# Performance work log

Hardware: AMD Instinct MI355X
Metric: run time of the kernel (lower is better)

## Reference

```python
import jax, jax.numpy as jnp
import numpy as np

N, E, G = 100000, 3_200_000, 128   # nodes, edges, graphs in batch
IN, H, C = 16, 64, 4               # in_dim, hidden, num_classes


def setup_inputs() -> dict:
    key = jax.random.key(0)
    ks = jax.random.split(key, 6)
    x = jax.random.normal(ks[0], (N, IN), dtype=jnp.float32)
    edge_index = jax.random.randint(ks[1], (2, E), 0, N, dtype=jnp.int64)
    batch = jnp.sort(jax.random.randint(ks[2], (N,), 0, G, dtype=jnp.int64))
    glorot = lambda k, shp, fan: jax.random.normal(k, shp, jnp.float32) / np.sqrt(fan).astype(np.float32)
    return dict(
        x=x, edge_index=edge_index, batch=batch,
        W1=glorot(ks[3], (IN, H), IN), b1=jnp.zeros((H,), jnp.float32),
        W2=glorot(ks[4], (H, H), H), b2=jnp.zeros((H,), jnp.float32),
        Wl=glorot(ks[5], (H, C), H), bl=jnp.zeros((C,), jnp.float32),
    )


def gcn_conv(x, src, dst, W, b, n):
    """PyG GCNConv: h = D^{-1/2} (A+I) D^{-1/2} (x W) + b, edges incl. self-loops."""
    h = x @ W  # [n, out]
    deg = jax.ops.segment_sum(jnp.ones(src.shape[0], x.dtype), dst, num_segments=n)
    dinv = jnp.where(deg > 0, jax.lax.rsqrt(deg), 0.0)
    norm = dinv[src] * dinv[dst]                       # [E+n]
    out = jax.ops.segment_sum(h[src] * norm[:, None], dst, num_segments=n)
    return out + b


def reference(x, edge_index, batch, W1, b1, W2, b2, Wl, bl):
    n = x.shape[0]
    loops = jnp.arange(n, dtype=edge_index.dtype)      # self-loops (gcn_norm)
    src = jnp.concatenate([edge_index[0], loops])
    dst = jnp.concatenate([edge_index[1], loops])
    h = jax.nn.relu(gcn_conv(x, src, dst, W1, b1, n))
    h = jax.nn.relu(gcn_conv(h, src, dst, W2, b2, n))
    g = jax.ops.segment_sum(h, batch, num_segments=G)  # global_add_pool -> [G, H]
    return g @ Wl + bl                                  # [G, C]
```

## Files before the change

kernel.cpp:

```cpp
#include <hip/hip_runtime.h>
#include <hip/hip_bf16.h>

#define NN 100000
#define EE 3200000
#define GG 128
#define IN_DIM 16
#define HDIM 64
#define CDIM 4

#define RN 256
#define NB ((NN + RN - 1) / RN)
#define CH 8192

typedef unsigned short u16;
typedef unsigned int u32;
typedef __attribute__((ext_vector_type(8))) short bf16x8;
typedef __attribute__((ext_vector_type(4))) float f32x4;

__device__ __forceinline__ float bf_lo(u32 w) { return __uint_as_float(w << 16); }
__device__ __forceinline__ float bf_hi(u32 w) { return __uint_as_float(w & 0xFFFF0000u); }
__device__ __forceinline__ u16 f2bf(float f) {
    u32 x = __float_as_uint(f);
    return (u16)((x + 0x7FFFu + ((x >> 16) & 1u)) >> 16);
}
__device__ __forceinline__ float rdlane(float v, int lane) {
    return __int_as_float(__builtin_amdgcn_readlane(__float_as_int(v), lane));
}


__global__ __launch_bounds__(512) void bhist_k(const int* __restrict__ dst,
                                               int* __restrict__ bcnt) {
    __shared__ int hist[NB];
    int t = threadIdx.x;
    long e0 = (long)blockIdx.x * CH;
    int cnt = (int)min((long)CH, (long)EE - e0);
    for (int i = t; i < NB; i += 512) hist[i] = 0;
    __syncthreads();
    for (int i = t; i < cnt; i += 512) atomicAdd(&hist[dst[e0 + i] >> 8], 1);
    __syncthreads();
    for (int i = t; i < NB; i += 512) {
        int v = hist[i];
        if (v > 0) atomicAdd(&bcnt[i], v);
    }
}

__global__ void bucketscan_k(const int* __restrict__ bcnt, int* __restrict__ bucketBase,
                             int* __restrict__ gcursor) {
    __shared__ int s[512];
    int t = threadIdx.x;
    int c = (t < NB) ? bcnt[t] : 0;
    s[t] = c;
    __syncthreads();
    for (int off = 1; off < 512; off <<= 1) {
        int v = (t >= off) ? s[t - off] : 0;
        __syncthreads();
        s[t] += v;
        __syncthreads();
    }
    if (t < NB) {
        int base = s[t] - c;
        bucketBase[t] = base;
        gcursor[t] = base;
    }
    if (t == 0) bucketBase[NB] = EE;
}


__global__ __launch_bounds__(512) void partition_k(const int* __restrict__ src,
                                                   const int* __restrict__ dst,
                                                   int* __restrict__ gcursor,
                                                   u32* __restrict__ pairs) {
    __shared__ int hist[NB];
    __shared__ int lbase[NB];
    __shared__ int gbase[NB];
    __shared__ int scanbuf[512];
    __shared__ u32 stag[CH];
    __shared__ u16 stagb[CH];
    int t = threadIdx.x;
    long e0 = (long)blockIdx.x * CH;
    int cnt = (int)min((long)CH, (long)EE - e0);

    for (int i = t; i < NB; i += 512) hist[i] = 0;
    __syncthreads();

    int myb[16], myloc[16];
    u32 myp[16];
#pragma unroll
    for (int r = 0; r < 16; ++r) {
        int i = t + (r << 9);
        if (i < cnt) {
            int s = src[e0 + i], d = dst[e0 + i];
            int b = d >> 8;
            myb[r] = b;
            myp[r] = ((u32)s << 8) | (u32)(d & 255);
            myloc[r] = atomicAdd(&hist[b], 1);
        } else {
            myb[r] = -1;
            myloc[r] = 0;
            myp[r] = 0;
        }
    }
    __syncthreads();

    scanbuf[t] = (t < NB) ? hist[t] : 0;
    __syncthreads();
    for (int off = 1; off < 512; off <<= 1) {
        int v = (t >= off) ? scanbuf[t - off] : 0;
        __syncthreads();
        scanbuf[t] += v;
        __syncthreads();
    }
    if (t < NB) {
        lbase[t] = scanbuf[t] - hist[t];
        gbase[t] = (hist[t] > 0) ? atomicAdd(&gcursor[t], hist[t]) : 0;
    }
    __syncthreads();

#pragma unroll
    for (int r = 0; r < 16; ++r) {
        if (myb[r] >= 0) {
            int pos = lbase[myb[r]] + myloc[r];
            stag[pos] = myp[r];
            stagb[pos] = (u16)myb[r];
        }
    }
    __syncthreads();

    for (int i = t; i < cnt; i += 512) {
        int b = stagb[i];
        pairs[gbase[b] + (i - lbase[b])] = stag[i];
    }
}


__global__ __launch_bounds__(512) void csrfill_k(const int* __restrict__ bucketBase,
                                                 const u32* __restrict__ pairs,
                                                 int* __restrict__ rowptr,
                                                 float* __restrict__ dinv,
                                                 int* __restrict__ srcS) {
    __shared__ int sb[256];
    __shared__ int sdeg[256];
    __shared__ int lcur[256];
    int b = blockIdx.x, t = threadIdx.x;
    int n0 = b << 8;
    int gb = bucketBase[b];
    int gend = bucketBase[b + 1];

    if (t < 256) sb[t] = 0;
    __syncthreads();

    for (int idx = gb + t; idx < gend; idx += 512) atomicAdd(&sb[pairs[idx] & 255u], 1);
    __syncthreads();

    int d = (t < 256) ? sb[t] : 0;
    if (t < 256) {
        sdeg[t] = d;
        int n = n0 + t;
        if (n < NN) dinv[n] = rsqrtf((float)(d + 1));
    }
    __syncthreads();
    for (int off = 1; off < 256; off <<= 1) {
        int v = 0;
        if (t < 256 && t >= off) v = sb[t - off];
        __syncthreads();
        if (t < 256) sb[t] += v;
        __syncthreads();
    }
    if (t < 256) {
        int excl = sb[t] - sdeg[t];
        int n = n0 + t;
        if (n < NN) rowptr[n] = gb + excl;
        lcur[t] = excl;
    }
    if (b == 0 && t == 0) rowptr[NN] = EE;
    __syncthreads();

    for (int idx = gb + t; idx < gend; idx += 512) {
        u32 p = pairs[idx];
        int dl = (int)(p & 255u);
        int slot = atomicAdd(&lcur[dl], 1);
        srcS[gb + slot] = (int)(p >> 8);
    }
}


__global__ void xs_k(const float* __restrict__ x, const float* __restrict__ dinv,
                     u16* __restrict__ xs) {
    int i = blockIdx.x * 256 + threadIdx.x;
    if (i >= NN * 4) return;
    int n = i >> 2;
    float dn = dinv[n];
    float4 v = ((const float4*)x)[i];
    u32 p0 = (u32)f2bf(v.x * dn) | ((u32)f2bf(v.y * dn) << 16);
    u32 p1 = (u32)f2bf(v.z * dn) | ((u32)f2bf(v.w * dn) << 16);
    uint2 pk; pk.x = p0; pk.y = p1;
    ((uint2*)xs)[i] = pk;
}

#define ACCUM8(acc, v)                       \
    {                                        \
        acc[0] += bf_lo(v.x);                \
        acc[1] += bf_hi(v.x);                \
        acc[2] += bf_lo(v.y);                \
        acc[3] += bf_hi(v.y);                \
        acc[4] += bf_lo(v.z);                \
        acc[5] += bf_hi(v.z);                \
        acc[6] += bf_lo(v.w);                \
        acc[7] += bf_hi(v.w);                \
    }

#define FOLD3(res, acc, mA, mB, mC)                                   \
    {                                                                 \
        float tj[4], uj[2];                                           \
        _Pragma("unroll")                                             \
        for (int j = 0; j < 4; j++) {                                 \
            float lo = acc[j], hi = acc[j + 4];                       \
            float snd = (lane & mA) ? lo : hi;                        \
            float rcv = __shfl_xor(snd, mA);                          \
            tj[j] = (lane & mA) ? hi + rcv : lo + rcv;                \
        }                                                             \
        _Pragma("unroll")                                             \
        for (int j = 0; j < 2; j++) {                                 \
            float lo = tj[j], hi = tj[j + 2];                         \
            float snd = (lane & mB) ? lo : hi;                        \
            float rcv = __shfl_xor(snd, mB);                          \
            uj[j] = (lane & mB) ? hi + rcv : lo + rcv;                \
        }                                                             \
        {                                                             \
            float lo = uj[0], hi = uj[1];                             \
            float snd = (lane & mC) ? lo : hi;                        \
            float rcv = __shfl_xor(snd, mC);                          \
            res = (lane & mC) ? hi + rcv : lo + rcv;                  \
        }                                                             \
    }


__global__ __launch_bounds__(256) void aggx_k(const u16* __restrict__ xs,
                                              const int* __restrict__ rowptr,
                                              const int* __restrict__ srcS,
                                              const float* __restrict__ dinv,
                                              const float* __restrict__ b1,
                                              const float* __restrict__ W1,
                                              u16* __restrict__ h1d) {
    int t = threadIdx.x;
    int lane = t & 63, w = t >> 6;
    int c = lane & 1, r = lane >> 1;
    int n0 = blockIdx.x * 8 + w * 2;
    int n1 = n0 + 1;

    float w1c[16];
#pragma unroll
    for (int k = 0; k < 16; k++) w1c[k] = W1[k * HDIM + lane];
    float b1l = b1[lane];

    int beg0 = rowptr[n0], end0 = rowptr[n0 + 1], end1 = rowptr[n0 + 2];
    int beg1 = end0;
    float dn0 = dinv[n0], dn1 = dinv[n1];

    float acc0[8] = {0, 0, 0, 0, 0, 0, 0, 0};
    float acc1[8] = {0, 0, 0, 0, 0, 0, 0, 0};
    if (r == 0) {
        uint4 v0 = *(const uint4*)(xs + ((size_t)n0 << 4) + (c << 3));
        uint4 v1 = *(const uint4*)(xs + ((size_t)n1 << 4) + (c << 3));
        ACCUM8(acc0, v0);
        ACCUM8(acc1, v1);
    }
    int itmax = max((end0 - beg0 + 31) >> 5, (end1 - beg1 + 31) >> 5);
    for (int it = 0; it < itmax; ++it) {
        int eA = beg0 + (it << 5) + r;
        int eB = beg1 + (it << 5) + r;
        int iA = srcS[eA < end0 ? eA : beg0];
        int iB = srcS[eB < end1 ? eB : beg1];
        uint4 vA = *(const uint4*)(xs + ((size_t)iA << 4) + (c << 3));
        uint4 vB = *(const uint4*)(xs + ((size_t)iB << 4) + (c << 3));
        if (eA < end0) ACCUM8(acc0, vA);
        if (eB < end1) ACCUM8(acc1, vB);
    }

    float v0, v1;
    FOLD3(v0, acc0, 2, 4, 8);
    FOLD3(v1, acc1, 2, 4, 8);
    v0 += __shfl_xor(v0, 16); v0 += __shfl_xor(v0, 32);
    v1 += __shfl_xor(v1, 16); v1 += __shfl_xor(v1, 32);

    float dot0 = 0.f, dot1 = 0.f;
#pragma unroll
    for (int k = 0; k < 16; k++) {
        int L = ((k >> 3) & 1) | (((k >> 2) & 1) << 1) | (((k >> 1) & 1) << 2) | ((k & 1) << 3);
        dot0 = fmaf(rdlane(v0, L), w1c[k], dot0);
        dot1 = fmaf(rdlane(v1, L), w1c[k], dot1);
    }
    float h0 = fmaxf(fmaf(dot0, dn0, b1l), 0.f);
    float h1 = fmaxf(fmaf(dot1, dn1, b1l), 0.f);

    h1d[(size_t)n0 * HDIM + lane] = f2bf(h0 * dn0);
    h1d[(size_t)n1 * HDIM + lane] = f2bf(h1 * dn1);
}


__global__ __launch_bounds__(256) void gemm_w2_k(const u16* __restrict__ h1d,
                                                 const float* __restrict__ W2,
                                                 u16* __restrict__ h2s) {
    int t = threadIdx.x;
    int lane = t & 63, w = t >> 6;
    int L4 = lane >> 4, L15 = lane & 15;

    bf16x8 bfrag[4][2];
#pragma unroll
    for (int nt = 0; nt < 4; ++nt)
#pragma unroll
        for (int s = 0; s < 2; ++s) {
#pragma unroll
            for (int j = 0; j < 8; ++j) {
                int k = s * 32 + L4 * 8 + j;
                bfrag[nt][s][j] = (short)f2bf(W2[k * HDIM + nt * 16 + L15]);
            }
        }

    int tile0 = (blockIdx.x * 4 + w) * 2;
#pragma unroll
    for (int ti = 0; ti < 2; ++ti) {
        int tile = tile0 + ti;
        if (tile >= NN / 16) break;
        int node = tile * 16 + L15;
        const u16* arow = h1d + (size_t)node * HDIM + L4 * 8;
        bf16x8 a0 = *(const bf16x8*)(arow);
        bf16x8 a1 = *(const bf16x8*)(arow + 32);

        f32x4 c[4];
#pragma unroll
        for (int nt = 0; nt < 4; ++nt) {
            c[nt] = (f32x4){0.f, 0.f, 0.f, 0.f};
            c[nt] = __builtin_amdgcn_mfma_f32_16x16x32_bf16(a0, bfrag[nt][0], c[nt], 0, 0, 0);
            c[nt] = __builtin_amdgcn_mfma_f32_16x16x32_bf16(a1, bfrag[nt][1], c[nt], 0, 0, 0);
        }
#pragma unroll
        for (int q = 0; q < 4; ++q) {
            int row = L4 * 4 + q;
            size_t base = (size_t)(tile * 16 + row) * HDIM + L15;
#pragma unroll
            for (int nt = 0; nt < 4; ++nt) h2s[base + nt * 16] = f2bf(c[nt][q]);
        }
    }
}


__global__ __launch_bounds__(512) void agg_pool_k(const u16* __restrict__ hs,
                                                  const int* __restrict__ rowptr,
                                                  const int* __restrict__ srcS,
                                                  const float* __restrict__ dinv,
                                                  const float* __restrict__ b2,
                                                  const int* __restrict__ batch,
                                                  float* __restrict__ g) {
    __shared__ float gacc[4][HDIM];
    __shared__ int s_g0, s_gmax;
    int t = threadIdx.x;
    int lane = t & 63, w = t >> 6;
    int nbase = blockIdx.x * 32;

    if (t < 4 * HDIM) gacc[t >> 6][t & 63] = 0.f;
    if (t == 0) { s_g0 = batch[nbase]; s_gmax = 0; }
    __syncthreads();
    int g0 = s_g0;

    int r = lane >> 3, c = lane & 7;
    int f = (c << 3) + ((lane & 8) ? 4 : 0) + ((lane & 16) ? 2 : 0) + ((lane & 32) ? 1 : 0);
    float b2f = b2[f];

    for (int ni = 0; ni < 4; ++ni) {
        int n = nbase + w * 4 + ni;
        int beg = rowptr[n], end = rowptr[n + 1];
        float acc[8] = {0.f, 0.f, 0.f, 0.f, 0.f, 0.f, 0.f, 0.f};
        if (r == 0) {
            uint4 v = *(const uint4*)(hs + ((size_t)n << 6) + (c << 3));
            ACCUM8(acc, v);
        }
        for (int e0 = beg; e0 < end; e0 += 32) {
            int eA = e0 + r, eB = eA + 8, eC = eA + 16, eD = eA + 24;
            int iA = srcS[eA < end ? eA : beg];
            int iB = srcS[eB < end ? eB : beg];
            int iC = srcS[eC < end ? eC : beg];
            int iD = srcS[eD < end ? eD : beg];
            uint4 vA = *(const uint4*)(hs + ((size_t)iA << 6) + (c << 3));
            uint4 vB = *(const uint4*)(hs + ((size_t)iB << 6) + (c << 3));
            uint4 vC = *(const uint4*)(hs + ((size_t)iC << 6) + (c << 3));
            uint4 vD = *(const uint4*)(hs + ((size_t)iD << 6) + (c << 3));
            if (eA < end) ACCUM8(acc, vA);
            if (eB < end) ACCUM8(acc, vB);
            if (eC < end) ACCUM8(acc, vC);
            if (eD < end) ACCUM8(acc, vD);
        }
        float red;
        FOLD3(red, acc, 8, 16, 32);
        float v = fmaf(red, dinv[n], b2f);
        v = fmaxf(v, 0.f);
        int gi = batch[n] - g0;
        if (gi < 4) {
            atomicAdd(&gacc[gi][f], v);
            if (lane == 0) atomicMax(&s_gmax, gi);
        } else {
            unsafeAtomicAdd(&g[(size_t)batch[n] * HDIM + f], v);
        }
    }
    __syncthreads();
    if (t < 4 * HDIM) {
        int slot = t >> 6, ff = t & 63;
        if (slot <= s_gmax) unsafeAtomicAdd(&g[(size_t)(g0 + slot) * HDIM + ff], gacc[slot][ff]);
    }
}

__global__ void final_k(const float* __restrict__ g, const float* __restrict__ Wl,
                        const float* __restrict__ bl, float* __restrict__ out) {
    int t = threadIdx.x;
    int gi = t >> 2, cc = t & 3;
    float acc = bl[cc];
#pragma unroll
    for (int k = 0; k < HDIM; k++) acc = fmaf(g[gi * HDIM + k], Wl[k * CDIM + cc], acc);
    out[gi * CDIM + cc] = acc;
}


extern "C" void kernel_launch(void* const* d_in, const int* in_sizes, int n_in,
                              void* d_out, int out_size, void* d_ws, size_t ws_size,
                              hipStream_t stream) {
    const float* x   = (const float*)d_in[0];
    const int*   ei  = (const int*)d_in[1];
    const int*   src = ei;
    const int*   dst = ei + EE;
    const int*   batch = (const int*)d_in[2];
    const float* W1 = (const float*)d_in[3];
    const float* b1 = (const float*)d_in[4];
    const float* W2 = (const float*)d_in[5];
    const float* b2 = (const float*)d_in[6];
    const float* Wl = (const float*)d_in[7];
    const float* bl = (const float*)d_in[8];
    float* out = (float*)d_out;

    char* w = (char*)d_ws;
    auto alloc = [&](size_t bytes) -> char* {
        char* p = w;
        w += (bytes + 255) & ~(size_t)255;
        return p;
    };
    int*   bcnt       = (int*)alloc((size_t)NB * 4);
    int*   bucketBase = (int*)alloc((size_t)(NB + 1) * 4);
    int*   gcursor    = (int*)alloc((size_t)NB * 4);
    u32*   pairs      = (u32*)alloc((size_t)EE * 4);
    int*   srcS       = (int*)alloc((size_t)EE * 4);
    int*   rowptr     = (int*)alloc((size_t)(NN + 1) * 4);
    float* dinv       = (float*)alloc((size_t)NN * 4);
    u16*   xs         = (u16*)alloc((size_t)NN * IN_DIM * 2);
    u16*   h1d        = (u16*)alloc((size_t)NN * HDIM * 2);
    u16*   h2s        = (u16*)alloc((size_t)NN * HDIM * 2);
    float* g          = (float*)alloc((size_t)GG * HDIM * 4);

    hipMemsetAsync(bcnt, 0, (size_t)NB * 4, stream);
    hipMemsetAsync(g, 0, (size_t)GG * HDIM * 4, stream);

    const int NCHUNK = (EE + CH - 1) / CH;
    bhist_k<<<NCHUNK, 512, 0, stream>>>(dst, bcnt);
    bucketscan_k<<<1, 512, 0, stream>>>(bcnt, bucketBase, gcursor);
    partition_k<<<NCHUNK, 512, 0, stream>>>(src, dst, gcursor, pairs);
    csrfill_k<<<NB, 512, 0, stream>>>(bucketBase, pairs, rowptr, dinv, srcS);

    xs_k<<<(NN * 4 + 255) / 256, 256, 0, stream>>>(x, dinv, xs);
    aggx_k<<<NN / 8, 256, 0, stream>>>(xs, rowptr, srcS, dinv, b1, W1, h1d);
    gemm_w2_k<<<(NN / 16 + 7) / 8, 256, 0, stream>>>(h1d, W2, h2s);
    agg_pool_k<<<(NN + 31) / 32, 512, 0, stream>>>(h2s, rowptr, srcS, dinv, b2, batch, g);
    final_k<<<1, 512, 0, stream>>>(g, Wl, bl, out);
}
```

Measured before the change: 179.2 us.

## Move W1 transform out of aggregation into fused MFMA W1+W2 MLP kernel

The layer-1 aggregation kernel now only gathers and sums the 16-dim input rows and writes a compact bf16 [N,16] buffer, dropping the per-lane readlane dot product with W1. A new kernel applies W1 by MFMA (K padded to 32, with bit-reversed row order to match the fold layout), adds bias, applies ReLU and dinv scaling, stages the result in LDS, then applies W2 by MFMA. This removes the 64-wide h1 round trip through global memory and the scalar dot-product work in the latency-bound gather kernel. It adds an extra bf16 rounding of the aggregate and some LDS traffic.

Result: slower. 185.3 us (+3.4%).

```diff
diff --git a/kernel.cpp b/kernel.cpp
--- a/kernel.cpp
+++ b/kernel.cpp
@@ -23,8 +23,8 @@
     u32 x = __float_as_uint(f);
     return (u16)((x + 0x7FFFu + ((x >> 16) & 1u)) >> 16);
 }
-__device__ __forceinline__ float rdlane(float v, int lane) {
-    return __int_as_float(__builtin_amdgcn_readlane(__float_as_int(v), lane));
+__device__ __forceinline__ int br4(int k) {
+    return ((k & 1) << 3) | ((k & 2) << 1) | ((k & 4) >> 1) | ((k & 8) >> 3);
 }
 
 
@@ -235,27 +235,18 @@
     }
 
 
-__global__ __launch_bounds__(256) void aggx_k(const u16* __restrict__ xs,
+__global__ __launch_bounds__(256) void aggs_k(const u16* __restrict__ xs,
                                               const int* __restrict__ rowptr,
                                               const int* __restrict__ srcS,
-                                              const float* __restrict__ dinv,
-                                              const float* __restrict__ b1,
-                                              const float* __restrict__ W1,
-                                              u16* __restrict__ h1d) {
+                                              u16* __restrict__ agg16) {
     int t = threadIdx.x;
     int lane = t & 63, w = t >> 6;
     int c = lane & 1, r = lane >> 1;
     int n0 = blockIdx.x * 8 + w * 2;
     int n1 = n0 + 1;
 
-    float w1c[16];
-#pragma unroll
-    for (int k = 0; k < 16; k++) w1c[k] = W1[k * HDIM + lane];
-    float b1l = b1[lane];
-
     int beg0 = rowptr[n0], end0 = rowptr[n0 + 1], end1 = rowptr[n0 + 2];
     int beg1 = end0;
-    float dn0 = dinv[n0], dn1 = dinv[n1];
 
     float acc0[8] = {0, 0, 0, 0, 0, 0, 0, 0};
     float acc1[8] = {0, 0, 0, 0, 0, 0, 0, 0};
@@ -283,29 +274,36 @@
     v0 += __shfl_xor(v0, 16); v0 += __shfl_xor(v0, 32);
     v1 += __shfl_xor(v1, 16); v1 += __shfl_xor(v1, 32);
 
-    float dot0 = 0.f, dot1 = 0.f;
-#pragma unroll
-    for (int k = 0; k < 16; k++) {
-        int L = ((k >> 3) & 1) | (((k >> 2) & 1) << 1) | (((k >> 1) & 1) << 2) | ((k & 1) << 3);
-        dot0 = fmaf(rdlane(v0, L), w1c[k], dot0);
-        dot1 = fmaf(rdlane(v1, L), w1c[k], dot1);
-    }
-    float h0 = fmaxf(fmaf(dot0, dn0, b1l), 0.f);
-    float h1 = fmaxf(fmaf(dot1, dn1, b1l), 0.f);
-
-    h1d[(size_t)n0 * HDIM + lane] = f2bf(h0 * dn0);
-    h1d[(size_t)n1 * HDIM + lane] = f2bf(h1 * dn1);
-}
-
-
-__global__ __launch_bounds__(256) void gemm_w2_k(const u16* __restrict__ h1d,
-                                                 const float* __restrict__ W2,
-                                                 u16* __restrict__ h2s) {
+    if (lane < 32) {
+        float v = (lane < 16) ? v0 : v1;
+        int n = (lane < 16) ? n0 : n1;
+        agg16[(size_t)n * 16 + (lane & 15)] = f2bf(v);
+    }
+}
+
+
+__global__ __launch_bounds__(256) void mlp_k(const u16* __restrict__ agg16,
+                                             const float* __restrict__ dinv,
+                                             const float* __restrict__ b1,
+                                             const float* __restrict__ W1,
+                                             const float* __restrict__ W2,
+                                             u16* __restrict__ h2s) {
+    __shared__ u16 atile[4][16][72];
     int t = threadIdx.x;
     int lane = t & 63, w = t >> 6;
     int L4 = lane >> 4, L15 = lane & 15;
 
-    bf16x8 bfrag[4][2];
+    bf16x8 w1frag[4];
+#pragma unroll
+    for (int nt = 0; nt < 4; ++nt) {
+#pragma unroll
+        for (int j = 0; j < 8; ++j) {
+            int k = L4 * 8 + j;
+            w1frag[nt][j] = (k < 16) ? (short)f2bf(W1[br4(k) * HDIM + nt * 16 + L15])
+                                     : (short)0;
+        }
+    }
+    bf16x8 w2frag[4][2];
 #pragma unroll
     for (int nt = 0; nt < 4; ++nt)
 #pragma unroll
@@ -313,33 +311,55 @@
 #pragma unroll
             for (int j = 0; j < 8; ++j) {
                 int k = s * 32 + L4 * 8 + j;
-                bfrag[nt][s][j] = (short)f2bf(W2[k * HDIM + nt * 16 + L15]);
+                w2frag[nt][s][j] = (short)f2bf(W2[k * HDIM + nt * 16 + L15]);
             }
         }
+    float b1l[4];
+#pragma unroll
+    for (int nt = 0; nt < 4; ++nt) b1l[nt] = b1[nt * 16 + L15];
 
     int tile0 = (blockIdx.x * 4 + w) * 2;
 #pragma unroll
     for (int ti = 0; ti < 2; ++ti) {
         int tile = tile0 + ti;
         if (tile >= NN / 16) break;
-        int node = tile * 16 + L15;
-        const u16* arow = h1d + (size_t)node * HDIM + L4 * 8;
-        bf16x8 a0 = *(const bf16x8*)(arow);
-        bf16x8 a1 = *(const bf16x8*)(arow + 32);
-
+        int row16 = tile * 16;
+
+        bf16x8 a = (bf16x8)(short)0;
+        if (L4 < 2) a = *(const bf16x8*)(agg16 + ((size_t)(row16 + L15) << 4) + L4 * 8);
         f32x4 c[4];
 #pragma unroll
         for (int nt = 0; nt < 4; ++nt) {
             c[nt] = (f32x4){0.f, 0.f, 0.f, 0.f};
-            c[nt] = __builtin_amdgcn_mfma_f32_16x16x32_bf16(a0, bfrag[nt][0], c[nt], 0, 0, 0);
-            c[nt] = __builtin_amdgcn_mfma_f32_16x16x32_bf16(a1, bfrag[nt][1], c[nt], 0, 0, 0);
-        }
+            c[nt] = __builtin_amdgcn_mfma_f32_16x16x32_bf16(a, w1frag[nt], c[nt], 0, 0, 0);
+        }
+        float dn[4];
+#pragma unroll
+        for (int q = 0; q < 4; ++q) dn[q] = dinv[row16 + L4 * 4 + q];
 #pragma unroll
         for (int q = 0; q < 4; ++q) {
             int row = L4 * 4 + q;
-            size_t base = (size_t)(tile * 16 + row) * HDIM + L15;
-#pragma unroll
-            for (int nt = 0; nt < 4; ++nt) h2s[base + nt * 16] = f2bf(c[nt][q]);
+#pragma unroll
+            for (int nt = 0; nt < 4; ++nt) {
+                float h = fmaxf(fmaf(c[nt][q], dn[q], b1l[nt]), 0.f) * dn[q];
+                atile[w][row][nt * 16 + L15] = f2bf(h);
+            }
+        }
+        bf16x8 a0 = *(const bf16x8*)&atile[w][L15][L4 * 8];
+        bf16x8 a1 = *(const bf16x8*)&atile[w][L15][L4 * 8 + 32];
+        f32x4 cc[4];
+#pragma unroll
+        for (int nt = 0; nt < 4; ++nt) {
+            cc[nt] = (f32x4){0.f, 0.f, 0.f, 0.f};
+            cc[nt] = __builtin_amdgcn_mfma_f32_16x16x32_bf16(a0, w2frag[nt][0], cc[nt], 0, 0, 0);
+            cc[nt] = __builtin_amdgcn_mfma_f32_16x16x32_bf16(a1, w2frag[nt][1], cc[nt], 0, 0, 0);
+        }
+#pragma unroll
+        for (int q = 0; q < 4; ++q) {
+            int row = L4 * 4 + q;
+            size_t base = (size_t)(row16 + row) * HDIM + L15;
+#pragma unroll
+            for (int nt = 0; nt < 4; ++nt) h2s[base + nt * 16] = f2bf(cc[nt][q]);
         }
     }
 }
@@ -450,7 +470,7 @@
     int*   rowptr     = (int*)alloc((size_t)(NN + 1) * 4);
     float* dinv       = (float*)alloc((size_t)NN * 4);
     u16*   xs         = (u16*)alloc((size_t)NN * IN_DIM * 2);
-    u16*   h1d        = (u16*)alloc((size_t)NN * HDIM * 2);
+    u16*   agg16      = (u16*)alloc((size_t)NN * 16 * 2);
     u16*   h2s        = (u16*)alloc((size_t)NN * HDIM * 2);
     float* g          = (float*)alloc((size_t)GG * HDIM * 4);
 
@@ -464,8 +484,8 @@
     csrfill_k<<<NB, 512, 0, stream>>>(bucketBase, pairs, rowptr, dinv, srcS);
 
     xs_k<<<(NN * 4 + 255) / 256, 256, 0, stream>>>(x, dinv, xs);
-    aggx_k<<<NN / 8, 256, 0, stream>>>(xs, rowptr, srcS, dinv, b1, W1, h1d);
-    gemm_w2_k<<<(NN / 16 + 7) / 8, 256, 0, stream>>>(h1d, W2, h2s);
-    agg_pool_k<<<(NN + 31) / 32, 512, 0, stream>>>(h2s, rowptr, srcS, dinv, b2, batch, g);
+    aggs_k<<<NN / 8, 256, 0, stream>>>(xs, rowptr, srcS, agg16);
+    mlp_k<<<(NN / 16 + 7) / 8, 256, 0, stream>>>(agg16, dinv, b1, W1, W2, h2s);
+    agg_pool_k<<<NN / 32, 512, 0, stream>>>(h2s, rowptr, srcS, dinv, b2, batch, g);
     final_k<<<1, 512, 0, stream>>>(g, Wl, bl, out);
 }
```
